# Kernel optimization log

Measured on AMD Instinct MI355X. Metric: run time of the kernel, lower is better.

## Reference

```python
import jax, jax.numpy as jnp
import numpy as np

B, L, H, W = 4, 16, 4096, 128   # W == nfeat == nclass (required by out.reshape)
NHID = 256

def setup_inputs() -> dict:
    key = jax.random.key(0)
    k1, k2, k3, k4 = jax.random.split(key, 4)
    x = jax.random.normal(k1, (B, L, H, W), dtype=jnp.float32)
    # row-normalized-ish dense adjacency stand-in for the sparse normalized adj
    adj = jax.random.uniform(k2, (H, H), dtype=jnp.float32) / H
    # GraphConvolution params: support = input @ Wk; out = adj @ support + bk
    W1 = jax.random.normal(k3, (W, NHID), dtype=jnp.float32) / np.sqrt(W)
    b1 = jnp.zeros((NHID,), dtype=jnp.float32)
    W2 = jax.random.normal(k4, (NHID, W), dtype=jnp.float32) / np.sqrt(NHID)
    b2 = jnp.zeros((W,), dtype=jnp.float32)
    return {"x": x, "adj": adj, "W1": W1, "b1": b1, "W2": W2, "b2": b2}

def reference(x, adj, W1, b1, W2, b2):
    Bv, Lv, Hv, Wv = x.shape
    xf = x.reshape(Bv * Lv, Hv, Wv)                      # [BL, H, F]
    # gc1: transform then aggregate, fused over all slices (replaces per-slice loop)
    h = jnp.einsum('nm,bmf->bnf', adj, xf @ W1) + b1     # [BL, H, nhid]
    h = jax.nn.relu(h)
    # dropout: inference mode (training=False) -> identity
    out = jnp.einsum('nm,bmf->bnf', adj, h @ W2) + b2    # [BL, H, nclass]
    out = out.reshape(Bv, Lv, Hv, Wv)
    return jax.nn.log_softmax(out, axis=-1)
```

## Files before the change

### kernel.cpp

```cpp
#include <hip/hip_runtime.h>

typedef __attribute__((ext_vector_type(4))) float f32x4;
typedef __attribute__((ext_vector_type(16))) float f32x16;
typedef __attribute__((ext_vector_type(4))) int i32x4;
typedef __attribute__((ext_vector_type(8))) int i32x8;
typedef union { i32x8 v8; i32x4 v4[2]; } opnd;

__device__ __forceinline__ unsigned fp4q(float v) {
  float a = __builtin_fabsf(v);
  unsigned q = (unsigned)(a > 0.25f) + (a > 0.75f) + (a > 1.25f) + (a > 1.75f)
             + (a > 2.5f) + (a > 3.5f) + (a > 5.0f);
  return q | (v < 0.0f ? 8u : 0u);
}

#if __has_builtin(__builtin_amdgcn_cvt_scalef32_pk_fp4_f32)
#define PKFP4(old, x, y, s) __builtin_amdgcn_cvt_scalef32_pk_fp4_f32((old), (x), (y), 1.0f, (s))
#else
#define PKFP4(old, x, y, s) ((old) | ((fp4q(x) | (fp4q(y) << 4)) << (8 * (s))))
#endif

__device__ __forceinline__ long tiled_addr(long r, long k, int nkb) {
  return (((r >> 5) * nkb) + (k >> 6)) * 2048 + ((k & 16) ? 1024 : 0)
       + (((r & 31) + (((k >> 5) & 1) << 5)) << 4) + (k & 15);
}
__device__ __forceinline__ long tile4_addr(long r, long k, int nkb) {
  return (((r >> 5) * nkb) + (k >> 6)) * 1024
       + (((r & 31) + (((k >> 5) & 1) << 5)) << 4) + ((k & 31) >> 1);
}

__device__ __forceinline__ long remap_wg(int lin, int nwg, int gx) {
  long g = lin;
  if ((nwg & 7) == 0) {
    int cpx = nwg >> 3;
    int gyx = cpx / gx;
    int xcd = lin & 7, idx = lin >> 3;
    if ((gx & 3) == 0 && gyx >= 4 && (gyx & 3) == 0) {
      int st = idx >> 4, wi = idx & 15;
      int nstr = gx >> 2;
      int str = st % nstr, stc = st / nstr;
      int r = str * 4 + (wi & 3);
      int c2 = stc * 4 + (wi >> 2);
      g = (long)xcd * cpx + (long)c2 * gx + r;
    } else {
      g = (long)xcd * cpx + idx;
    }
  }
  return g;
}

__global__ __launch_bounds__(256) void cvtAdj4t(const float* __restrict__ in,
                                                unsigned char* __restrict__ out, long n) {
  long i = ((long)blockIdx.x * 256 + threadIdx.x) * 8;
  if (i >= n) return;
  float4 a = *(const float4*)(in + i);
  float4 b = *(const float4*)(in + i + 4);
  const float S = 24576.0f;
  unsigned word = PKFP4(0u, a.x * S, a.y * S, 0);
  word = PKFP4(word, a.z * S, a.w * S, 1);
  word = PKFP4(word, b.x * S, b.y * S, 2);
  word = PKFP4(word, b.z * S, b.w * S, 3);
  long r = i >> 12;
  long k = i & 4095;
  *(int*)(out + tile4_addr(r, k, 64)) = (int)word;
}

__global__ __launch_bounds__(256) void cvtX4t(const float* __restrict__ X,
                                              unsigned char* __restrict__ out4) {
  __shared__ float tile[32][33];
  const int tid = threadIdx.x;
  const long bl = blockIdx.z;
  const int m0 = blockIdx.y * 32;
  const int w0 = blockIdx.x * 32;
  const float* xb = X + (bl * 4096 + m0) * 128 + w0;
  int row = tid >> 3, cg = tid & 7;
  float4 v = *(const float4*)(xb + (long)row * 128 + cg * 4);
  tile[row][cg * 4 + 0] = v.x;
  tile[row][cg * 4 + 1] = v.y;
  tile[row][cg * 4 + 2] = v.z;
  tile[row][cg * 4 + 3] = v.w;
  __syncthreads();
  if (tid < 128) {
    int wv = tid & 31, mg = tid >> 5;
    float t[8];
#pragma unroll
    for (int i = 0; i < 8; ++i) t[i] = tile[mg * 8 + i][wv];
    unsigned word = PKFP4(0u, t[0], t[1], 0);
    word = PKFP4(word, t[2], t[3], 1);
    word = PKFP4(word, t[4], t[5], 2);
    word = PKFP4(word, t[6], t[7], 3);
    long r = bl * 128 + w0 + wv;
    long k = m0 + mg * 8;
    *(int*)(out4 + tile4_addr(r, k, 64)) = (int)word;
  }
}

__global__ __launch_bounds__(256) void prep_params(const float* __restrict__ W1,
                                                   const float* __restrict__ W2,
                                                   unsigned char* __restrict__ W1T8,
                                                   unsigned char* __restrict__ W2T8) {
  int idx = blockIdx.x * 256 + threadIdx.x;
  if (idx < 32768) {
    int f = idx >> 7, wv = idx & 127;
    float v = W1[wv * 256 + f] * 16.0f;
    int pk = __builtin_amdgcn_cvt_pk_fp8_f32(v, v, 0, 0);
    W1T8[tiled_addr(f, wv, 2)] = (unsigned char)(pk & 0xff);
  } else {
    int t = idx - 32768;
    int cc = t >> 8, f = t & 255;
    float v = W2[f * 128 + cc] * 16.0f;
    int pk = __builtin_amdgcn_cvt_pk_fp8_f32(v, v, 0, 0);
    W2T8[tiled_addr(cc, f, 4)] = (unsigned char)(pk & 0xff);
  }
}

__global__ __launch_bounds__(256, 3) void gemmS1(const unsigned char* __restrict__ A4,
                                                 const unsigned char* __restrict__ X4,
                                                 const unsigned char* __restrict__ W1T8,
                                                 const unsigned char* __restrict__ W2T8,
                                                 unsigned char* __restrict__ t2T4,
                                                 const float* __restrict__ b1,
                                                 int K, int gx) {
  __shared__ unsigned char S1buf[16384];
  __shared__ unsigned char hbuf[32768];
  __shared__ float b1s[256];
  const int tid = threadIdx.x;
  const int l = tid & 63;
  const int w = tid >> 6;
  b1s[tid] = b1[tid] * 128.0f;
  long g = remap_wg(blockIdx.x, gridDim.x, gx);
  const long row0 = (g % gx) * 128;
  const long bl = g / gx;
  const int nkb = K >> 6;
  const int wr = w >> 1, wc = w & 1;
  const unsigned char* pA = A4 + (((row0 >> 5) + wr * 2) * (long)nkb) * 1024 + l * 16;
  const unsigned char* pB = X4 + ((bl * 4 + wc * 2) * (long)nkb) * 1024 + l * 16;

  f32x16 acc[2][2] = {};
  opnd aA[2], bA[2], aB[2], bB[2], aC[2], bC[2], aD[2], bD[2];
  const i32x4 z4 = {0, 0, 0, 0};
#pragma unroll
  for (int fi = 0; fi < 2; ++fi) {
    aA[fi].v4[1] = z4; aB[fi].v4[1] = z4; aC[fi].v4[1] = z4; aD[fi].v4[1] = z4;
    bA[fi].v4[1] = z4; bB[fi].v4[1] = z4; bC[fi].v4[1] = z4; bD[fi].v4[1] = z4;
  }

#define LOADG(KT, AV, BV) do { long off_ = (long)(KT) * 1024;                         \
    _Pragma("unroll") for (int fi = 0; fi < 2; ++fi)                                  \
      AV[fi].v4[0] = *(const i32x4*)(pA + (long)fi * nkb * 1024 + off_);              \
    _Pragma("unroll") for (int j = 0; j < 2; ++j)                                     \
      BV[j].v4[0] = *(const i32x4*)(pB + (long)j * nkb * 1024 + off_);                \
  } while (0)

#define MFMAS(AV, BV) do {                                                            \
    __builtin_amdgcn_s_setprio(1);                                                    \
    _Pragma("unroll") for (int fi = 0; fi < 2; ++fi)                                  \
      _Pragma("unroll") for (int j = 0; j < 2; ++j)                                   \
        acc[fi][j] = __builtin_amdgcn_mfma_scale_f32_32x32x64_f8f6f4(                 \
            BV[j].v8, AV[fi].v8, acc[fi][j], 4, 4, 0, 127, 0, 124);                   \
    __builtin_amdgcn_s_setprio(0); } while (0)

  const int nkt = K >> 6;
  LOADG(0, aA, bA); LOADG(1, aB, bB); LOADG(2, aC, bC);
  int kt = 0;
  for (; kt + 7 < nkt; kt += 4) {
    LOADG(kt + 3, aD, bD); MFMAS(aA, bA);
    LOADG(kt + 4, aA, bA); MFMAS(aB, bB);
    LOADG(kt + 5, aB, bB); MFMAS(aC, bC);
    LOADG(kt + 6, aC, bC); MFMAS(aD, bD);
  }
  LOADG(nkt - 1, aD, bD);
  MFMAS(aA, bA); MFMAS(aB, bB); MFMAS(aC, bC); MFMAS(aD, bD);
#undef LOADG
#undef MFMAS

  const int hi = l >> 5;
  const int ln = l & 31;
#pragma unroll
  for (int fi = 0; fi < 2; ++fi) {
    int n = (wr * 2 + fi) * 32 + ln;
#pragma unroll
    for (int j = 0; j < 2; ++j) {
      int wb = (wc * 2 + j) * 32 + 4 * hi;
#pragma unroll
      for (int r4 = 0; r4 < 4; ++r4) {
        int w0 = wb + 8 * r4;
        int word = __builtin_amdgcn_cvt_pk_fp8_f32(acc[fi][j][4 * r4 + 0],
                                                   acc[fi][j][4 * r4 + 1], 0, false);
        word = __builtin_amdgcn_cvt_pk_fp8_f32(acc[fi][j][4 * r4 + 2],
                                               acc[fi][j][4 * r4 + 3], word, true);
        *(int*)(S1buf + tiled_addr(n, w0, 2)) = word;
      }
    }
  }
  __syncthreads();

  const float c1 = 128.0f / 49152.0f;
#pragma unroll
  for (int hh = 0; hh < 2; ++hh) {
#pragma unroll
    for (int fi = 0; fi < 2; ++fi)
#pragma unroll
      for (int jb = 0; jb < 2; ++jb) acc[fi][jb] = (f32x16){};
#pragma unroll
    for (int kt1 = 0; kt1 < 2; ++kt1) {
#pragma unroll
      for (int jb = 0; jb < 2; ++jb) {
        opnd aw;
        const unsigned char* pW = W1T8 + (long)((hh * 4 + wc * 2 + jb) * 2 + kt1) * 2048 + l * 16;
        aw.v4[0] = *(const i32x4*)(pW);
        aw.v4[1] = *(const i32x4*)(pW + 1024);
#pragma unroll
        for (int fi = 0; fi < 2; ++fi) {
          opnd bs;
          const unsigned char* pS = S1buf + (long)((wr * 2 + fi) * 2 + kt1) * 2048 + l * 16;
          bs.v4[0] = *(const i32x4*)(pS);
          bs.v4[1] = *(const i32x4*)(pS + 1024);
          acc[fi][jb] = __builtin_amdgcn_mfma_scale_f32_32x32x64_f8f6f4(
              aw.v8, bs.v8, acc[fi][jb], 0, 0, 0, 127, 0, 127);
        }
      }
    }
#pragma unroll
    for (int jb = 0; jb < 2; ++jb) {
      int fb = (hh * 4 + wc * 2 + jb) * 32 + 4 * hi;
#pragma unroll
      for (int r4 = 0; r4 < 4; ++r4) {
        int f0 = fb + 8 * r4;
        float4 bb = *(const float4*)(b1s + f0);
#pragma unroll
        for (int fi = 0; fi < 2; ++fi) {
          int n = (wr * 2 + fi) * 32 + ln;
          float v0 = fmaxf(fmaf(acc[fi][jb][4 * r4 + 0], c1, bb.x), 0.0f);
          float v1 = fmaxf(fmaf(acc[fi][jb][4 * r4 + 1], c1, bb.y), 0.0f);
          float v2 = fmaxf(fmaf(acc[fi][jb][4 * r4 + 2], c1, bb.z), 0.0f);
          float v3 = fmaxf(fmaf(acc[fi][jb][4 * r4 + 3], c1, bb.w), 0.0f);
          int word = __builtin_amdgcn_cvt_pk_fp8_f32(v0, v1, 0, false);
          word = __builtin_amdgcn_cvt_pk_fp8_f32(v2, v3, word, true);
          *(int*)(hbuf + tiled_addr(n, f0, 4)) = word;
        }
      }
    }
  }
  __syncthreads();

#pragma unroll
  for (int fi = 0; fi < 2; ++fi)
#pragma unroll
    for (int jb = 0; jb < 2; ++jb) acc[fi][jb] = (f32x16){};
#pragma unroll
  for (int kt2 = 0; kt2 < 4; ++kt2) {
#pragma unroll
    for (int jb = 0; jb < 2; ++jb) {
      opnd bw;
      const unsigned char* pW = W2T8 + (long)((wc * 2 + jb) * 4 + kt2) * 2048 + l * 16;
      bw.v4[0] = *(const i32x4*)(pW);
      bw.v4[1] = *(const i32x4*)(pW + 1024);
#pragma unroll
      for (int fi = 0; fi < 2; ++fi) {
        opnd ah;
        const unsigned char* pH = hbuf + (long)((wr * 2 + fi) * 4 + kt2) * 2048 + l * 16;
        ah.v4[0] = *(const i32x4*)(pH);
        ah.v4[1] = *(const i32x4*)(pH + 1024);
        acc[fi][jb] = __builtin_amdgcn_mfma_scale_f32_32x32x64_f8f6f4(
            ah.v8, bw.v8, acc[fi][jb], 0, 0, 0, 127, 0, 127);
      }
    }
  }
  unsigned char* ob = t2T4 + bl * 262144;
#pragma unroll
  for (int fi = 0; fi < 2; ++fi) {
#pragma unroll
    for (int jb = 0; jb < 2; ++jb) {
      int cc = wc * 64 + jb * 32 + ln;
#pragma unroll
      for (int run = 0; run < 4; ++run) {
        long n0 = row0 + wr * 64 + fi * 32 + 8 * run + 4 * hi;
        const float s = 0.125f;
        unsigned pkw = PKFP4(0u, acc[fi][jb][run * 4 + 0] * s,
                                 acc[fi][jb][run * 4 + 1] * s, 0);
        pkw = PKFP4(pkw, acc[fi][jb][run * 4 + 2] * s,
                         acc[fi][jb][run * 4 + 3] * s, 1);
        *(ushort*)(ob + tile4_addr(cc, n0, 64)) = (ushort)pkw;
      }
    }
  }
}

__global__ __launch_bounds__(512) void gemm256sm(const unsigned char* __restrict__ A4,
                                                 const unsigned char* __restrict__ B4,
                                                 float* __restrict__ out,
                                                 const float* __restrict__ bias,
                                                 float ooScale, int K, int gx,
                                                 int chunkBase) {
  __shared__ unsigned char ring[65536];
  const int tid = threadIdx.x;
  const int l = tid & 63;
  const int w = tid >> 6;
  int lin = blockIdx.x;
  const int nwg = gridDim.x;
  if (gx == 16 && (nwg & 63) == 0) {
    int xcd = lin & 7, idx = lin >> 3;
    int cpg = nwg >> 6;
    int r = ((xcd & 1) << 3) + (idx & 7);
    int c = (xcd >> 1) * cpg + (idx >> 3);
    lin = c * gx + r;
  } else if ((nwg & 7) == 0) {
    int cpx = nwg >> 3;
    lin = (lin & 7) * cpx + (lin >> 3);
  }
  const long row0 = (long)(lin % gx) * 256;
  const long col0 = (long)(lin / gx) * 256;
  const int nkb = K >> 6;
  const unsigned char* sBp = B4 + (((col0 >> 5) + w) * (long)nkb) * 1024 + l * 16;
  unsigned char* ringw = ring + w * 1024;
  const unsigned char* ringr = ring + ((w & 1) * 4) * 1024 + l * 16;
  const unsigned char* pA = A4 + (((row0 + (w >> 1) * 64) >> 5) * (long)nkb) * 1024 + l * 16;

  f32x16 acc[2][4] = {};
  opnd bv[4], a0v[2], a1v[2], a2v[2], a3v[2];
  const i32x4 z4 = {0, 0, 0, 0};
#pragma unroll
  for (int j = 0; j < 4; ++j) bv[j].v4[1] = z4;
#pragma unroll
  for (int fi = 0; fi < 2; ++fi) {
    a0v[fi].v4[1] = z4; a1v[fi].v4[1] = z4; a2v[fi].v4[1] = z4; a3v[fi].v4[1] = z4;
  }

#define STGB(KT) __builtin_amdgcn_global_load_lds(                                    \
    (const unsigned int*)(const void*)(sBp + (long)(KT) * 1024),                      \
    (unsigned int*)(ringw + (((KT) & 7) << 13)), 16, 0, 0)
#define LOADA(KT, AV) do { long o_ = (long)(KT) * 1024;                               \
    AV[0].v4[0] = *(const i32x4*)(pA + o_);                                           \
    AV[1].v4[0] = *(const i32x4*)(pA + (long)nkb * 1024 + o_); } while (0)
#define LDB(KT) do { const unsigned char* p_ = ringr + (((KT) & 7) << 13);            \
    bv[0].v4[0] = *(const i32x4*)(p_);                                                \
    bv[1].v4[0] = *(const i32x4*)(p_ + 1024);                                         \
    bv[2].v4[0] = *(const i32x4*)(p_ + 2048);                                         \
    bv[3].v4[0] = *(const i32x4*)(p_ + 3072); } while (0)
#define MFMAS(AV) do { __builtin_amdgcn_s_setprio(1);                                 \
    _Pragma("unroll") for (int fi = 0; fi < 2; ++fi)                                  \
      _Pragma("unroll") for (int j = 0; j < 4; ++j)                                   \
        acc[fi][j] = __builtin_amdgcn_mfma_scale_f32_32x32x64_f8f6f4(                 \
            AV[fi].v8, bv[j].v8, acc[fi][j], 4, 4, 0, 127, 0, 127);                   \
    __builtin_amdgcn_s_setprio(0); } while (0)
#define BODY(KT, N, DOSTG, DOA, ALD, AUSE) do {                                       \
    LDB(KT);                                                                          \
    if (DOA) LOADA((KT) + 3, ALD);                                                    \
    if (DOSTG) STGB((KT) + 6);                                                        \
    asm volatile("s_waitcnt vmcnt(" N ")" ::: "memory");                              \
    MFMAS(AUSE);                                                                      \
    __builtin_amdgcn_s_barrier(); } while (0)

  const int nkt = K >> 6;
  LOADA(0, a0v); LOADA(1, a1v); LOADA(2, a2v);
  STGB(0); STGB(1); STGB(2); STGB(3); STGB(4); STGB(5);
  asm volatile("s_waitcnt vmcnt(5)" ::: "memory");
  __builtin_amdgcn_s_barrier();

  BODY(0, "7", 1, 1, a3v, a0v);
  BODY(1, "9", 1, 1, a0v, a1v);
  BODY(2, "11", 1, 1, a1v, a2v);
  for (int kt = 3; kt + 9 <= nkt - 1; kt += 4) {
    BODY(kt,     "10", 1, 1, a2v, a3v);
    BODY(kt + 1, "10", 1, 1, a3v, a0v);
    BODY(kt + 2, "10", 1, 1, a0v, a1v);
    BODY(kt + 3, "10", 1, 1, a1v, a2v);
  }
  BODY(55, "10", 1, 1, a2v, a3v);
  BODY(56, "10", 1, 1, a3v, a0v);
  BODY(57, "10", 1, 1, a0v, a1v);
  BODY(58, "9",  0, 1, a1v, a2v);
  BODY(59, "8",  0, 1, a2v, a3v);
  BODY(60, "7",  0, 1, a3v, a0v);
  BODY(61, "4",  0, 0, a0v, a1v);
  BODY(62, "2",  0, 0, a0v, a2v);
  BODY(63, "0",  0, 0, a0v, a3v);
#undef STGB
#undef LOADA
#undef LDB
#undef MFMAS
#undef BODY

  const int hi = l >> 5;
  const int bl = (int)(col0 >> 7) + (w & 1);
  float bb[4];
#pragma unroll
  for (int j = 0; j < 4; ++j) bb[j] = bias[j * 32 + (l & 31)];
#pragma unroll
  for (int fi = 0; fi < 2; ++fi) {
#pragma unroll
    for (int rr = 0; rr < 16; ++rr) {
      float v0 = acc[fi][0][rr] * ooScale + bb[0];
      float v1 = acc[fi][1][rr] * ooScale + bb[1];
      float v2 = acc[fi][2][rr] * ooScale + bb[2];
      float v3 = acc[fi][3][rr] * ooScale + bb[3];
      float m = fmaxf(fmaxf(v0, v1), fmaxf(v2, v3));
#pragma unroll
      for (int o = 16; o > 0; o >>= 1) m = fmaxf(m, __shfl_xor(m, o));
      float s = __expf(v0 - m) + __expf(v1 - m) + __expf(v2 - m) + __expf(v3 - m);
#pragma unroll
      for (int o = 16; o > 0; o >>= 1) s += __shfl_xor(s, o);
      float lse = m + __logf(s);
      long row = row0 + (w >> 1) * 64 + fi * 32 + ((rr & 3) + 8 * (rr >> 2) + 4 * hi);
      float* dst = out + ((long)(chunkBase + bl) * 4096 + row) * 128;
      dst[(l & 31)] = v0 - lse;
      dst[32 + (l & 31)] = v1 - lse;
      dst[64 + (l & 31)] = v2 - lse;
      dst[96 + (l & 31)] = v3 - lse;
    }
  }
}

extern "C" void kernel_launch(void* const* d_in, const int* in_sizes, int n_in,
                              void* d_out, int out_size, void* d_ws, size_t ws_size,
                              hipStream_t stream) {
  const float* x = (const float*)d_in[0];
  const float* adj = (const float*)d_in[1];
  const float* W1 = (const float*)d_in[2];
  const float* b1 = (const float*)d_in[3];
  const float* W2 = (const float*)d_in[4];
  const float* b2 = (const float*)d_in[5];
  float* out = (float*)d_out;
  char* ws = (char*)d_ws;

  unsigned char* adj4 = (unsigned char*)ws;
  unsigned char* W1T8 = (unsigned char*)(ws + 8388608);
  unsigned char* W2T8 = (unsigned char*)(ws + 8388608 + 32768);
  const size_t base = 9ull * 1024 * 1024;

  const int cands[6] = {64, 32, 16, 8, 4, 2};
  int c = 2;
  for (int t = 0; t < 6; ++t) {
    size_t need = base + (size_t)cands[t] * 524288;
    if (need <= ws_size) { c = cands[t]; break; }
  }
  unsigned char* x4T = (unsigned char*)(ws + base);
  unsigned char* t2T4 = x4T + (size_t)c * 262144;

  cvtAdj4t<<<8192, 256, 0, stream>>>(adj, adj4, (long)4096 * 4096);
  prep_params<<<256, 256, 0, stream>>>(W1, W2, W1T8, W2T8);

  int chunks = 64 / c;
  for (int cb = 0; cb < chunks; ++cb) {
    int base_bl = cb * c;
    const float* xc = x + (long)base_bl * 4096 * 128;

    cvtX4t<<<dim3(4, 128, c), 256, 0, stream>>>(xc, x4T);
    gemmS1<<<32 * c, 256, 0, stream>>>(adj4, x4T, W1T8, W2T8, t2T4, b1, 4096, 32);
    gemm256sm<<<16 * (c / 2), 512, 0, stream>>>(adj4, t2T4, out, b2,
                                                1.0f / 6291456.0f, 4096, 16, base_bl);
  }
}
```

Baseline: 233.3 us.

## Stage gemmS1 main-loop operands through LDS with async global_load_lds triple buffering

The main K loop of gemmS1 no longer has each wave load its own A and X fragments straight from global memory into registers. Each wave now issues global_load_lds for one 32-row slab into a shared, triple-buffered LDS ring, and fragments are read back from LDS, so waves sharing a row or column slab do not load it twice. The S1/h buffers alias the same LDS region after the loop, and the bias is read from global memory and scaled inline instead of being staged in LDS. Risks are extra barriers per K step, a hardcoded trip count of 32 K-blocks (K fixed at 4096), and higher LDS use, which may reduce occupancy.

```diff
diff --git a/kernel.cpp b/kernel.cpp
--- a/kernel.cpp
+++ b/kernel.cpp
@@ -120,58 +120,79 @@
                                                  unsigned char* __restrict__ t2T4,
                                                  const float* __restrict__ b1,
                                                  int K, int gx) {
-  __shared__ unsigned char S1buf[16384];
-  __shared__ unsigned char hbuf[32768];
-  __shared__ float b1s[256];
+  __shared__ unsigned char lds[49152];
   const int tid = threadIdx.x;
   const int l = tid & 63;
   const int w = tid >> 6;
-  b1s[tid] = b1[tid] * 128.0f;
   long g = remap_wg(blockIdx.x, gridDim.x, gx);
   const long row0 = (g % gx) * 128;
   const long bl = g / gx;
   const int nkb = K >> 6;
   const int wr = w >> 1, wc = w & 1;
-  const unsigned char* pA = A4 + (((row0 >> 5) + wr * 2) * (long)nkb) * 1024 + l * 16;
-  const unsigned char* pB = X4 + ((bl * 4 + wc * 2) * (long)nkb) * 1024 + l * 16;
+  const unsigned char* sAp = A4 + (((row0 >> 5) + w) * (long)nkb) * 1024 + l * 16;
+  const unsigned char* sXp = X4 + ((bl * 4 + w) * (long)nkb) * 1024 + l * 16;
+  unsigned char* ldsw = lds + w * 1024;
+  const unsigned char* rA = lds + (wr * 2) * 1024 + l * 16;
+  const unsigned char* rX = lds + 4096 + (wc * 2) * 1024 + l * 16;
 
   f32x16 acc[2][2] = {};
-  opnd aA[2], bA[2], aB[2], bB[2], aC[2], bC[2], aD[2], bD[2];
+  opnd aE[2], xE[2], aO[2], xO[2];
   const i32x4 z4 = {0, 0, 0, 0};
 #pragma unroll
   for (int fi = 0; fi < 2; ++fi) {
-    aA[fi].v4[1] = z4; aB[fi].v4[1] = z4; aC[fi].v4[1] = z4; aD[fi].v4[1] = z4;
-    bA[fi].v4[1] = z4; bB[fi].v4[1] = z4; bC[fi].v4[1] = z4; bD[fi].v4[1] = z4;
-  }
-
-#define LOADG(KT, AV, BV) do { long off_ = (long)(KT) * 1024;                         \
-    _Pragma("unroll") for (int fi = 0; fi < 2; ++fi)                                  \
-      AV[fi].v4[0] = *(const i32x4*)(pA + (long)fi * nkb * 1024 + off_);              \
-    _Pragma("unroll") for (int j = 0; j < 2; ++j)                                     \
-      BV[j].v4[0] = *(const i32x4*)(pB + (long)j * nkb * 1024 + off_);                \
+    aE[fi].v4[1] = z4; xE[fi].v4[1] = z4;
+    aO[fi].v4[1] = z4; xO[fi].v4[1] = z4;
+  }
+
+#define STG(B, SL) do { long o0_ = (long)(2 * (B)) * 1024; long o1_ = o0_ + 1024;     \
+    unsigned char* d_ = ldsw + (SL) * 16384;                                          \
+    __builtin_amdgcn_global_load_lds((const unsigned int*)(const void*)(sAp + o0_),   \
+                                     (unsigned int*)(d_), 16, 0, 0);                  \
+    __builtin_amdgcn_global_load_lds((const unsigned int*)(const void*)(sXp + o0_),   \
+                                     (unsigned int*)(d_ + 4096), 16, 0, 0);           \
+    __builtin_amdgcn_global_load_lds((const unsigned int*)(const void*)(sAp + o1_),   \
+                                     (unsigned int*)(d_ + 8192), 16, 0, 0);           \
+    __builtin_amdgcn_global_load_lds((const unsigned int*)(const void*)(sXp + o1_),   \
+                                     (unsigned int*)(d_ + 12288), 16, 0, 0);          \
   } while (0)
-
-#define MFMAS(AV, BV) do {                                                            \
+#define LDF(SL, HALF, AV, XV) do { const long s_ = (SL) * 16384 + (HALF) * 8192;      \
+    AV[0].v4[0] = *(const i32x4*)(rA + s_);                                           \
+    AV[1].v4[0] = *(const i32x4*)(rA + s_ + 1024);                                    \
+    XV[0].v4[0] = *(const i32x4*)(rX + s_);                                           \
+    XV[1].v4[0] = *(const i32x4*)(rX + s_ + 1024); } while (0)
+#define MFMAS(AV, XV) do {                                                            \
     __builtin_amdgcn_s_setprio(1);                                                    \
     _Pragma("unroll") for (int fi = 0; fi < 2; ++fi)                                  \
       _Pragma("unroll") for (int j = 0; j < 2; ++j)                                   \
         acc[fi][j] = __builtin_amdgcn_mfma_scale_f32_32x32x64_f8f6f4(                 \
-            BV[j].v8, AV[fi].v8, acc[fi][j], 4, 4, 0, 127, 0, 124);                   \
+            XV[j].v8, AV[fi].v8, acc[fi][j], 4, 4, 0, 127, 0, 124);                   \
     __builtin_amdgcn_s_setprio(0); } while (0)
-
-  const int nkt = K >> 6;
-  LOADG(0, aA, bA); LOADG(1, aB, bB); LOADG(2, aC, bC);
-  int kt = 0;
-  for (; kt + 7 < nkt; kt += 4) {
-    LOADG(kt + 3, aD, bD); MFMAS(aA, bA);
-    LOADG(kt + 4, aA, bA); MFMAS(aB, bB);
-    LOADG(kt + 5, aB, bB); MFMAS(aC, bC);
-    LOADG(kt + 6, aC, bC); MFMAS(aD, bD);
-  }
-  LOADG(nkt - 1, aD, bD);
-  MFMAS(aA, bA); MFMAS(aB, bB); MFMAS(aC, bC); MFMAS(aD, bD);
-#undef LOADG
+#define BODY(SL, SS, DOSTG, B, N) do {                                                \
+    LDF(SL, 0, aE, xE);                                                               \
+    if (DOSTG) STG((B) + 2, SS);                                                      \
+    LDF(SL, 1, aO, xO);                                                               \
+    MFMAS(aE, xE);                                                                    \
+    MFMAS(aO, xO);                                                                    \
+    asm volatile("s_waitcnt vmcnt(" N ")" ::: "memory");                              \
+    __builtin_amdgcn_s_barrier(); } while (0)
+
+  STG(0, 0); STG(1, 1);
+  asm volatile("s_waitcnt vmcnt(4)" ::: "memory");
+  __builtin_amdgcn_s_barrier();
+  for (int b = 0; b < 30; b += 3) {
+    BODY(0, 2, 1, b + 0, "4");
+    BODY(1, 0, 1, b + 1, "4");
+    BODY(2, 1, 1, b + 2, "4");
+  }
+  BODY(0, 0, 0, 30, "0");
+  BODY(1, 0, 0, 31, "0");
+#undef STG
+#undef LDF
 #undef MFMAS
+#undef BODY
+
+  unsigned char* S1buf = lds;
+  unsigned char* hbuf = lds + 16384;
 
   const int hi = l >> 5;
   const int ln = l & 31;
@@ -226,14 +247,14 @@
 #pragma unroll
       for (int r4 = 0; r4 < 4; ++r4) {
         int f0 = fb + 8 * r4;
-        float4 bb = *(const float4*)(b1s + f0);
+        float4 bb = *(const float4*)(b1 + f0);
 #pragma unroll
         for (int fi = 0; fi < 2; ++fi) {
           int n = (wr * 2 + fi) * 32 + ln;
-          float v0 = fmaxf(fmaf(acc[fi][jb][4 * r4 + 0], c1, bb.x), 0.0f);
-          float v1 = fmaxf(fmaf(acc[fi][jb][4 * r4 + 1], c1, bb.y), 0.0f);
-          float v2 = fmaxf(fmaf(acc[fi][jb][4 * r4 + 2], c1, bb.z), 0.0f);
-          float v3 = fmaxf(fmaf(acc[fi][jb][4 * r4 + 3], c1, bb.w), 0.0f);
+          float v0 = fmaxf(fmaf(acc[fi][jb][4 * r4 + 0], c1, bb.x * 128.0f), 0.0f);
+          float v1 = fmaxf(fmaf(acc[fi][jb][4 * r4 + 1], c1, bb.y * 128.0f), 0.0f);
+          float v2 = fmaxf(fmaf(acc[fi][jb][4 * r4 + 2], c1, bb.z * 128.0f), 0.0f);
+          float v3 = fmaxf(fmaf(acc[fi][jb][4 * r4 + 3], c1, bb.w * 128.0f), 0.0f);
           int word = __builtin_amdgcn_cvt_pk_fp8_f32(v0, v1, 0, false);
           word = __builtin_amdgcn_cvt_pk_fp8_f32(v2, v3, word, true);
           *(int*)(hbuf + tiled_addr(n, f0, 4)) = word;
```

After: 229.9 us. Within noise of the previous version (-1.5%).
